# Optimization experiments

Measured on AMD Instinct MI355X. Metric: run time of the kernel, lower is better.

The kernel has to match this reference:

```python
import jax, jax.numpy as jnp
import numpy as np

K_NEIGHBORS = 3
CLASSES = 5


def _l2_norm(x):
    # x: (N, C, H, W) -> (N, H*W, C), unit L2 norm over channel dim
    N, C, H, W = x.shape
    x = x.reshape(N, C, H * W).transpose(0, 2, 1)
    return x / jnp.linalg.norm(x, axis=-1, keepdims=True)


def setup_inputs() -> dict:
    key = jax.random.key(0)
    k1, k2 = jax.random.split(key)
    anchor = jax.random.normal(k1, (32, 64, 21, 21), dtype=jnp.float32)
    support_set = jax.random.normal(k2, (25, 64, 21, 21), dtype=jnp.float32)
    return {"anchor": anchor, "support_set": support_set, "av_num": 1, "sav_num": 1}


def reference(anchor, support_set, av_num, sav_num):
    # anchor: (B*AV, C, H, W), support_set: (L*S, C, H, W)
    q = _l2_norm(anchor)            # (B, HW, C)
    s = _l2_norm(support_set)       # (L*S, HW, C)
    C = s.shape[-1]
    s_flat = s.reshape(-1, C)       # (M, C), M = L*S*HW (class-major)
    # dense cosine similarity: (B, HW, M)
    sim = jnp.einsum('bqc,mc->bqm', q, s_flat)
    B, HW, M = sim.shape
    per_cls = M // CLASSES
    # (B//av, av, HW, L, S*HW)
    sim = sim.reshape(B // av_num, av_num, HW, CLASSES, per_cls)
    sim = jax.nn.sigmoid(sim)
    # av_num == 1 -> squeeze AV dim (matches torch squeeze(1) path)
    sim = sim[:, 0] if av_num == 1 else jnp.power(jnp.prod(sim, axis=1), 1.0 / av_num)
    # per-class top-k over descriptors, sum over k and over query locations
    topk = jax.lax.top_k(sim, K_NEIGHBORS)[0]        # (B, HW, L, K)
    i2c_sim = topk.sum(axis=-1).sum(axis=-2)         # (B, L)
    return i2c_sim
```

## Files before the change

### kernel.cpp

```cpp
#include <hip/hip_runtime.h>
#include <hip/hip_bf16.h>
#include <math.h>

#define CLASSES     5
#define C_DIM       64
#define HW          441
#define B_ANCH      32
#define NSUP        25
#define NROWS       (B_ANCH*HW)
#define MSUP        (NSUP*HW)
#define PER_CLS     (MSUP/CLASSES)
#define TILE_COLS   32
#define TILE_BYTES  (TILE_COLS*ROW_BYTES)
#define PER_CLS_PAD 2304
#define NPAD        (PER_CLS_PAD - PER_CLS)
#define ROW_BYTES   (C_DIM*2)
#define QUARTERS    4
#define TILES_PER_Q 18
#define ROWS_PER_BLK 128
#define NBLK_X      ((NROWS + ROWS_PER_BLK - 1) / ROWS_PER_BLK)

#define NEG_INF  (-1e30f)

typedef __bf16 bf16x8 __attribute__((ext_vector_type(8)));
typedef float  f32x4  __attribute__((ext_vector_type(4)));

#define TOP3_INS(v, t0, t1, t2) do {                              \
    float _v = (v);                                               \
    float _n0 = fmaxf(_v, (t0));                                  \
    float _n1 = __builtin_amdgcn_fmed3f(_v, (t0), (t1));          \
    float _n2 = __builtin_amdgcn_fmed3f(_v, (t1), (t2));          \
    (t0) = _n0; (t1) = _n1; (t2) = _n2; } while (0)

#define TRIPLE_MERGE(u0, u1, u2, v0, v1, v2) do {                 \
    float _A = fminf((u0), (v0));                                 \
    float _B = fmaxf((u1), (v1));                                 \
    float _E = fmaxf((u2), (v2));                                 \
    float _m0 = fmaxf((u0), (v0));                                \
    float _m1 = __builtin_amdgcn_fmed3f((u0), (v0), _B);          \
    float _m2 = __builtin_amdgcn_fmed3f(_A, _B, _E);              \
    (u0) = _m0; (u1) = _m1; (u2) = _m2; } while (0)

typedef __attribute__((address_space(1))) const void g_void;
typedef __attribute__((address_space(3))) void l_void;
__device__ __forceinline__ void gload_lds16(const void* g, void* l) {
    __builtin_amdgcn_global_load_lds((g_void*)g, (l_void*)l, 16, 0, 0);
}

__global__ __launch_bounds__(256) void norm_rows_kernel(
    const float* __restrict__ anchor, const float* __restrict__ support,
    __bf16* __restrict__ qb, __bf16* __restrict__ sb) {
    int r = blockIdx.x * 256 + threadIdx.x;
    const int total_main = MSUP + NROWS;
    if (r >= total_main) {
        int i = r - total_main;
        if (i < CLASSES * NPAD) {
            int cls = i / NPAD, ix = PER_CLS + i % NPAD;
            __bf16* op = sb + ((size_t)cls * PER_CLS_PAD + ix) * C_DIM;
            bf16x8 z = {};
            #pragma unroll
            for (int c0 = 0; c0 < C_DIM; c0 += 8) *(bf16x8*)(op + c0) = z;
        }
        return;
    }
    bool isSup = r < MSUP;
    int rc = isSup ? r : r - MSUP;
    const float* in = isSup ? support : anchor;
    int img = rc / HW, p = rc % HW;
    const float* base = in + (size_t)img * C_DIM * HW + p;
    float q[C_DIM];
    float ss = 0.f;
    #pragma unroll
    for (int c = 0; c < C_DIM; ++c) { q[c] = base[c * HW]; ss += q[c] * q[c]; }
    float sc = rsqrtf(ss);
    __bf16* op;
    if (isSup) {
        int cls = rc / PER_CLS, ix = rc - cls * PER_CLS;
        op = sb + ((size_t)cls * PER_CLS_PAD + ix) * C_DIM;
    } else {
        op = qb + (size_t)rc * C_DIM;
    }
    #pragma unroll
    for (int c0 = 0; c0 < C_DIM; c0 += 8) {
        bf16x8 v;
        #pragma unroll
        for (int j = 0; j < 8; ++j) v[j] = (__bf16)(q[c0 + j] * sc);
        *(bf16x8*)(op + c0) = v;
    }
}

template<int QNT, bool TAIL>
__device__ __forceinline__ void gemm_quarter(
    const char* qbase,
    char* smem_base,
    int laneOff,
    int pr0, int lane, int lr,
    const bf16x8 a0[2], const bf16x8 a1[2],
    float t0[2][4], float t1[2][4], float t2[2][4]) {

    auto stage = [&](int buf, int tt) {
        const char* tb = qbase + tt * TILE_BYTES;
        int pr = pr0;
        gload_lds16(tb + ((pr >> 1) * 2048 + (pr & 1) * 64) + laneOff,
                    smem_base + buf * 4096 + pr * 1024);
    };

    const bf16x8* sm = (const bf16x8*)smem_base;
    const f32x4 z = {0.f, 0.f, 0.f, 0.f};

    stage(0, 0);
    stage(1, 1);
    #pragma unroll
    for (int tt = 0; tt < QNT; ++tt) {
        if (tt < QNT - 1) asm volatile("s_waitcnt vmcnt(1)" ::: "memory");
        else              asm volatile("s_waitcnt vmcnt(0)" ::: "memory");
        __builtin_amdgcn_s_barrier();
        if (tt + 2 < QNT) stage((tt + 2) % 3, tt + 2);
        const int buf = tt % 3;
        const bool tail = TAIL && (tt == QNT - 1);
        bf16x8 b[4];
        #pragma unroll
        for (int s = 0; s < 2; ++s) {
            b[2*s]   = sm[((buf*2 + s)*2 + 0)*64 + lane];
            b[2*s+1] = sm[((buf*2 + s)*2 + 1)*64 + lane];
        }
        f32x4 acc[4];
        __builtin_amdgcn_s_setprio(1);
        #pragma unroll
        for (int s = 0; s < 2; ++s)
            #pragma unroll
            for (int r = 0; r < 2; ++r) {
                acc[s*2+r] = __builtin_amdgcn_mfma_f32_16x16x32_bf16(
                    a0[r], b[2*s], z, 0, 0, 0);
                acc[s*2+r] = __builtin_amdgcn_mfma_f32_16x16x32_bf16(
                    a1[r], b[2*s+1], acc[s*2+r], 0, 0, 0);
            }
        __builtin_amdgcn_s_setprio(0);
        if (!tail) {
            #pragma unroll
            for (int s = 0; s < 2; ++s)
                #pragma unroll
                for (int r = 0; r < 2; ++r)
                    #pragma unroll
                    for (int j = 0; j < 4; ++j)
                        TOP3_INS(acc[s*2+r][j], t0[r][j], t1[r][j], t2[r][j]);
        } else {
            #pragma unroll
            for (int s = 0; s < 2; ++s) {
                bool valid = (s == 0) || (lr < 13);
                #pragma unroll
                for (int r = 0; r < 2; ++r)
                    #pragma unroll
                    for (int j = 0; j < 4; ++j) {
                        float v = valid ? acc[s*2+r][j] : NEG_INF;
                        TOP3_INS(v, t0[r][j], t1[r][j], t2[r][j]);
                    }
            }
        }
    }
}

__global__ __launch_bounds__(256, 4) void knn_mfma_kernel(
    const __bf16* __restrict__ qb, const __bf16* __restrict__ sb,
    float* __restrict__ part) {
    __shared__ bf16x8 smem[3][2][2][64];

    int lane = threadIdx.x & 63;
    int w    = threadIdx.x >> 6;
    int lr   = lane & 15;
    int kg   = lane >> 4;
    int cls  = blockIdx.y >> 2;
    int q    = blockIdx.y & 3;
    int rowbase = blockIdx.x * ROWS_PER_BLK + w * 32;

    bf16x8 a0[2], a1[2];
    #pragma unroll
    for (int r = 0; r < 2; ++r) {
        int arow = rowbase + r * 16 + lr;
        int arc  = arow < NROWS ? arow : NROWS - 1;
        const bf16x8* qrow = (const bf16x8*)(qb + (size_t)arc * C_DIM);
        a0[r] = qrow[kg];
        a1[r] = qrow[4 + kg];
    }

    float t0[2][4], t1[2][4], t2[2][4];
    #pragma unroll
    for (int r = 0; r < 2; ++r)
        #pragma unroll
        for (int j = 0; j < 4; ++j) {
            t0[r][j] = NEG_INF; t1[r][j] = NEG_INF; t2[r][j] = NEG_INF;
        }

    const char* qbase = (const char*)sb
        + (size_t)cls * PER_CLS_PAD * ROW_BYTES
        + (size_t)q * TILES_PER_Q * TILE_BYTES;
    int laneOff = lr * ROW_BYTES + kg * 16;

    if (q == 3)
        gemm_quarter<15, true >(qbase, (char*)smem, laneOff, w, lane, lr,
                                a0, a1, t0, t1, t2);
    else
        gemm_quarter<18, false>(qbase, (char*)smem, laneOff, w, lane, lr,
                                a0, a1, t0, t1, t2);

    #pragma unroll
    for (int r = 0; r < 2; ++r) {
        #pragma unroll
        for (int j = 0; j < 4; ++j) {
            float u0 = t0[r][j], u1 = t1[r][j], u2 = t2[r][j];
            #pragma unroll
            for (int off = 1; off < 16; off <<= 1) {
                float v0 = __shfl_xor(u0, off, 64);
                float v1 = __shfl_xor(u1, off, 64);
                float v2 = __shfl_xor(u2, off, 64);
                TRIPLE_MERGE(u0, u1, u2, v0, v1, v2);
            }
            int row = rowbase + r * 16 + kg * 4 + j;
            if (lr == 0 && row < NROWS) {
                float* pp = part +
                    ((size_t)(row * CLASSES + cls) * QUARTERS + q) * 3;
                pp[0] = u0; pp[1] = u1; pp[2] = u2;
            }
        }
    }
}

__global__ __launch_bounds__(64) void merge_reduce_kernel(
    const float* __restrict__ part, float* __restrict__ out) {
    int bl = blockIdx.x;
    int b = bl / CLASSES;
    int l = bl % CLASSES;
    int lane = threadIdx.x;
    float acc = 0.f;
    for (int p = lane; p < HW; p += 64) {
        int row = b * HW + p;
        const float* pp = part + (size_t)(row * CLASSES + l) * (QUARTERS * 3);
        float u0 = pp[0], u1 = pp[1], u2 = pp[2];
        TRIPLE_MERGE(u0, u1, u2, pp[3], pp[4],  pp[5]);
        TRIPLE_MERGE(u0, u1, u2, pp[6], pp[7],  pp[8]);
        TRIPLE_MERGE(u0, u1, u2, pp[9], pp[10], pp[11]);
        acc += 1.f / (1.f + __expf(-u0))
             + 1.f / (1.f + __expf(-u1))
             + 1.f / (1.f + __expf(-u2));
    }
    #pragma unroll
    for (int off = 32; off; off >>= 1) acc += __shfl_xor(acc, off, 64);
    if (lane == 0) out[bl] = acc;
}

extern "C" void kernel_launch(void* const* d_in, const int* in_sizes, int n_in,
                              void* d_out, int out_size, void* d_ws, size_t ws_size,
                              hipStream_t stream) {
    const float* anchor  = (const float*)d_in[0];
    const float* support = (const float*)d_in[1];

    __bf16* sb = (__bf16*)d_ws;
    __bf16* qb = sb + (size_t)CLASSES * PER_CLS_PAD * C_DIM;
    float* part = (float*)(qb + (size_t)NROWS * C_DIM);

    {
        int total = MSUP + NROWS + CLASSES * NPAD;
        dim3 g((total + 255) / 256);
        norm_rows_kernel<<<g, 256, 0, stream>>>(anchor, support, qb, sb);
    }
    {
        dim3 g(NBLK_X, CLASSES * QUARTERS);
        knn_mfma_kernel<<<g, 256, 0, stream>>>(qb, sb, part);
    }
    {
        dim3 gm(B_ANCH * CLASSES);
        merge_reduce_kernel<<<gm, 64, 0, stream>>>(part, (float*)d_out);
    }
}
```

Baseline: 55.22 us.

## Give each wave a private double-buffered LDS region and drop block barriers

Each wave now stages the whole support tile into its own private double-buffered LDS slice with four async global-to-LDS loads, instead of sharing one triple-buffered tile loaded cooperatively by all four waves. This removes the per-tile block-wide s_barrier so waves progress independently. In exchange every wave loads the same support data, which quadruples global/L2 load traffic and raises LDS use from 6 KB to 32 KB per block, which could limit occupancy at 4 blocks per CU.

```diff
diff --git a/kernel.cpp b/kernel.cpp
--- a/kernel.cpp
+++ b/kernel.cpp
@@ -11,10 +11,10 @@
 #define MSUP        (NSUP*HW)
 #define PER_CLS     (MSUP/CLASSES)
 #define TILE_COLS   32
+#define ROW_BYTES   (C_DIM*2)
 #define TILE_BYTES  (TILE_COLS*ROW_BYTES)
 #define PER_CLS_PAD 2304
 #define NPAD        (PER_CLS_PAD - PER_CLS)
-#define ROW_BYTES   (C_DIM*2)
 #define QUARTERS    4
 #define TILES_PER_Q 18
 #define ROWS_PER_BLK 128
@@ -46,6 +46,8 @@
 __device__ __forceinline__ void gload_lds16(const void* g, void* l) {
     __builtin_amdgcn_global_load_lds((g_void*)g, (l_void*)l, 16, 0, 0);
 }
+
+#define MFMA16(A, B, C) __builtin_amdgcn_mfma_f32_16x16x32_bf16((A), (B), (C), 0, 0, 0)
 
 __global__ __launch_bounds__(256) void norm_rows_kernel(
     const float* __restrict__ anchor, const float* __restrict__ support,
@@ -90,71 +92,64 @@
 }
 
 template<int QNT, bool TAIL>
-__device__ __forceinline__ void gemm_quarter(
+__device__ __forceinline__ void scan_quarter(
     const char* qbase,
-    char* smem_base,
-    int laneOff,
-    int pr0, int lane, int lr,
+    char* myLds,
+    int lane, int lr,
     const bf16x8 a0[2], const bf16x8 a1[2],
     float t0[2][4], float t1[2][4], float t2[2][4]) {
 
     auto stage = [&](int buf, int tt) {
         const char* tb = qbase + tt * TILE_BYTES;
-        int pr = pr0;
-        gload_lds16(tb + ((pr >> 1) * 2048 + (pr & 1) * 64) + laneOff,
-                    smem_base + buf * 4096 + pr * 1024);
+        #pragma unroll
+        for (int pr = 0; pr < 4; ++pr)
+            gload_lds16(tb + (pr >> 1) * 2048 + (pr & 1) * 64,
+                        myLds + buf * 4096 + pr * 1024);
     };
 
-    const bf16x8* sm = (const bf16x8*)smem_base;
     const f32x4 z = {0.f, 0.f, 0.f, 0.f};
 
     stage(0, 0);
     stage(1, 1);
     #pragma unroll
     for (int tt = 0; tt < QNT; ++tt) {
-        if (tt < QNT - 1) asm volatile("s_waitcnt vmcnt(1)" ::: "memory");
+        if (tt < QNT - 1) asm volatile("s_waitcnt vmcnt(4)" ::: "memory");
         else              asm volatile("s_waitcnt vmcnt(0)" ::: "memory");
-        __builtin_amdgcn_s_barrier();
-        if (tt + 2 < QNT) stage((tt + 2) % 3, tt + 2);
-        const int buf = tt % 3;
+        const int buf = tt & 1;
+        const bf16x8* sm = (const bf16x8*)(myLds + buf * 4096);
+        bf16x8 b0 = sm[0 * 64 + lane];
+        bf16x8 b1 = sm[1 * 64 + lane];
+        bf16x8 b2 = sm[2 * 64 + lane];
+        bf16x8 b3 = sm[3 * 64 + lane];
+        asm volatile("s_waitcnt lgkmcnt(0)" ::: "memory");
+        __builtin_amdgcn_sched_barrier(0);
+        if (tt + 2 < QNT) stage(buf, tt + 2);
+        f32x4 acc0, acc1, acc2, acc3;
+        __builtin_amdgcn_s_setprio(1);
+        acc0 = MFMA16(a0[0], b0, z); acc0 = MFMA16(a1[0], b1, acc0);
+        acc1 = MFMA16(a0[1], b0, z); acc1 = MFMA16(a1[1], b1, acc1);
+        acc2 = MFMA16(a0[0], b2, z); acc2 = MFMA16(a1[0], b3, acc2);
+        acc3 = MFMA16(a0[1], b2, z); acc3 = MFMA16(a1[1], b3, acc3);
+        __builtin_amdgcn_s_setprio(0);
         const bool tail = TAIL && (tt == QNT - 1);
-        bf16x8 b[4];
-        #pragma unroll
-        for (int s = 0; s < 2; ++s) {
-            b[2*s]   = sm[((buf*2 + s)*2 + 0)*64 + lane];
-            b[2*s+1] = sm[((buf*2 + s)*2 + 1)*64 + lane];
-        }
-        f32x4 acc[4];
-        __builtin_amdgcn_s_setprio(1);
-        #pragma unroll
-        for (int s = 0; s < 2; ++s)
-            #pragma unroll
-            for (int r = 0; r < 2; ++r) {
-                acc[s*2+r] = __builtin_amdgcn_mfma_f32_16x16x32_bf16(
-                    a0[r], b[2*s], z, 0, 0, 0);
-                acc[s*2+r] = __builtin_amdgcn_mfma_f32_16x16x32_bf16(
-                    a1[r], b[2*s+1], acc[s*2+r], 0, 0, 0);
-            }
-        __builtin_amdgcn_s_setprio(0);
         if (!tail) {
             #pragma unroll
-            for (int s = 0; s < 2; ++s)
-                #pragma unroll
-                for (int r = 0; r < 2; ++r)
-                    #pragma unroll
-                    for (int j = 0; j < 4; ++j)
-                        TOP3_INS(acc[s*2+r][j], t0[r][j], t1[r][j], t2[r][j]);
+            for (int j = 0; j < 4; ++j) {
+                TOP3_INS(acc0[j], t0[0][j], t1[0][j], t2[0][j]);
+                TOP3_INS(acc1[j], t0[1][j], t1[1][j], t2[1][j]);
+                TOP3_INS(acc2[j], t0[0][j], t1[0][j], t2[0][j]);
+                TOP3_INS(acc3[j], t0[1][j], t1[1][j], t2[1][j]);
+            }
         } else {
-            #pragma unroll
-            for (int s = 0; s < 2; ++s) {
-                bool valid = (s == 0) || (lr < 13);
-                #pragma unroll
-                for (int r = 0; r < 2; ++r)
-                    #pragma unroll
-                    for (int j = 0; j < 4; ++j) {
-                        float v = valid ? acc[s*2+r][j] : NEG_INF;
-                        TOP3_INS(v, t0[r][j], t1[r][j], t2[r][j]);
-                    }
+            bool valid = lr < 13;
+            #pragma unroll
+            for (int j = 0; j < 4; ++j) {
+                TOP3_INS(acc0[j], t0[0][j], t1[0][j], t2[0][j]);
+                TOP3_INS(acc1[j], t0[1][j], t1[1][j], t2[1][j]);
+                float v2 = valid ? acc2[j] : NEG_INF;
+                float v3 = valid ? acc3[j] : NEG_INF;
+                TOP3_INS(v2, t0[0][j], t1[0][j], t2[0][j]);
+                TOP3_INS(v3, t0[1][j], t1[1][j], t2[1][j]);
             }
         }
     }
@@ -163,7 +158,7 @@
 __global__ __launch_bounds__(256, 4) void knn_mfma_kernel(
     const __bf16* __restrict__ qb, const __bf16* __restrict__ sb,
     float* __restrict__ part) {
-    __shared__ bf16x8 smem[3][2][2][64];
+    __shared__ char smem[4][8192];
 
     int lane = threadIdx.x & 63;
     int w    = threadIdx.x >> 6;
@@ -193,15 +188,13 @@
 
     const char* qbase = (const char*)sb
         + (size_t)cls * PER_CLS_PAD * ROW_BYTES
-        + (size_t)q * TILES_PER_Q * TILE_BYTES;
-    int laneOff = lr * ROW_BYTES + kg * 16;
+        + (size_t)q * TILES_PER_Q * TILE_BYTES
+        + lr * ROW_BYTES + kg * 16;
 
     if (q == 3)
-        gemm_quarter<15, true >(qbase, (char*)smem, laneOff, w, lane, lr,
-                                a0, a1, t0, t1, t2);
+        scan_quarter<15, true >(qbase, smem[w], lane, lr, a0, a1, t0, t1, t2);
     else
-        gemm_quarter<18, false>(qbase, (char*)smem, laneOff, w, lane, lr,
-                                a0, a1, t0, t1, t2);
+        scan_quarter<18, false>(qbase, smem[w], lane, lr, a0, a1, t0, t1, t2);
 
     #pragma unroll
     for (int r = 0; r < 2; ++r) {
```

After: 94.95 us. 72.0% more time.
